# Optimization experiments

Measured on AMD Instinct MI355X. Metric: run time of the kernel, lower is better.

The kernel has to match this reference:

```python
import jax, jax.numpy as jnp
import numpy as np

TOP_K = 8
SCALE = 2.5  # moe_router_scaling_factor
EPS = 1e-20


def setup_inputs() -> dict:
    key = jax.random.key(0)
    k1, k2 = jax.random.split(key)
    B, S, H, E = 4, 4096, 4096, 64
    hidden_states = jax.random.normal(k1, (B, S, H), dtype=jnp.float32)
    gate_weight = jax.random.normal(k2, (E, H), dtype=jnp.float32) * 0.02
    router_bias = jnp.zeros((E,), dtype=jnp.float32)
    return {"hidden_states": hidden_states, "gate_weight": gate_weight, "router_bias": router_bias}


def reference(hidden_states, gate_weight, router_bias):
    B, S, H = hidden_states.shape
    x = hidden_states.reshape(-1, H).astype(jnp.float32)  # [T, H]
    # need_fp32_gate: fp32 matmul against gate weight transpose -> [T, E]
    logits = jnp.einsum('th,eh->te', x, gate_weight.astype(jnp.float32))
    gate_prob = jax.nn.sigmoid(logits)
    biased = gate_prob + router_bias[None, :]
    # topk on bias-shifted probs; weights gathered from UNbiased probs
    _, indices = jax.lax.top_k(biased, TOP_K)                       # [T, K]
    topk_prob = jnp.take_along_axis(gate_prob, indices, axis=1)     # [T, K]
    weights = topk_prob / (jnp.sum(topk_prob, axis=-1, keepdims=True) + EPS)
    weights = weights * SCALE
    return weights, indices
```

## Files before the change

kernel.cpp:

```cpp
#include <hip/hip_runtime.h>
#include <cmath>


typedef float f32x4 __attribute__((ext_vector_type(4)));
typedef short s16x8 __attribute__((ext_vector_type(8)));
typedef unsigned int u32;
typedef u32 u32x4 __attribute__((ext_vector_type(4)));

#define E_DIM 64
#define KC 32
#define CH_BYTES 12288
#define NPART 4
#define HI_OFF (2u << 20)

union V16 { u32x4 u; s16x8 s; };

__device__ __forceinline__ unsigned short f2bf(float f) {
  unsigned u = __float_as_uint(f);
  u += 0x7fffu + ((u >> 16) & 1u);
  return (unsigned short)(u >> 16);
}
__device__ __forceinline__ float bf2f(unsigned short s) {
  return __uint_as_float(((unsigned)s) << 16);
}

__global__ __launch_bounds__(256) void split_w(
    const float* __restrict__ w, unsigned char* __restrict__ w3, int Hdim)
{
  const int kpr = Hdim >> 4;
  const int g = blockIdx.x * 256 + threadIdx.x;
  const int e = g / kpr;
  const int k0 = (g - e * kpr) * 16;
  if (e >= E_DIM) return;

  const float* src = w + (size_t)e * Hdim + k0;
  float f[16];
#pragma unroll
  for (int i = 0; i < 4; ++i) {
    float4 v = *(const float4*)(src + i * 4);
    f[i*4+0] = v.x; f[i*4+1] = v.y; f[i*4+2] = v.z; f[i*4+3] = v.w;
  }
  unsigned short hs[16], ms[16], ls[16];
#pragma unroll
  for (int i = 0; i < 16; ++i) {
    unsigned short h = f2bf(f[i]);
    float r1 = f[i] - bf2f(h);
    unsigned short m = f2bf(r1);
    float r2 = r1 - bf2f(m);
    hs[i] = h; ms[i] = m; ls[i] = f2bf(r2);
  }
  const int c  = k0 >> 5;
  const int n  = e >> 4;
  const int la = (e & 15) + (((k0 & 31) >> 3) << 4);
  unsigned char* base = w3 + (size_t)c * CH_BYTES + n * 1024;

#define STORE_SPLIT(arr, s)                                              \
  do {                                                                   \
    s16x8 pa, pb;                                                        \
    _Pragma("unroll")                                                    \
    for (int j = 0; j < 8; ++j) { pa[j] = (short)arr[j]; pb[j] = (short)arr[8+j]; } \
    *(s16x8*)(base + (s)*4096 + la * 16)        = pa;                    \
    *(s16x8*)(base + (s)*4096 + (la + 16) * 16) = pb;                    \
  } while (0)

  STORE_SPLIT(hs, 0);
  STORE_SPLIT(ms, 1);
  STORE_SPLIT(ls, 2);
#undef STORE_SPLIT
}

__global__ __launch_bounds__(256, 3) void router_mfma(
    const float* __restrict__ x, const unsigned char* __restrict__ w3,
    const float* __restrict__ bias, float* __restrict__ outw,
    float* __restrict__ outi, float* __restrict__ hi_p,
    float* __restrict__ lo_p, int T, int Hdim)
{
  __shared__ __align__(16) unsigned char lds[2][CH_BYTES];

  const int tid  = threadIdx.x;
  const int wid  = tid >> 6;
  const int lane = tid & 63;
  const int lc   = lane & 15;
  const int lq   = lane >> 4;
  const int by   = blockIdx.y;
  const int nch  = Hdim / KC / gridDim.y;
  const int t0   = blockIdx.x * 64;

  const float* xp = x + (size_t)(t0 + wid * 16 + lc) * Hdim
                      + (size_t)by * nch * KC + lq * 8;
  const unsigned char* w3p = w3 + (size_t)by * nch * CH_BYTES;

  f32x4 acc[4], sum_[4], comp[4];
#pragma unroll
  for (int n = 0; n < 4; ++n) {
    acc[n] = (f32x4){0,0,0,0};
    sum_[n] = (f32x4){0,0,0,0};
    comp[n] = (f32x4){0,0,0,0};
  }

#define WAITV2() asm volatile("s_waitcnt vmcnt(2)" ::: "memory")
#define WAITV0() asm volatile("s_waitcnt vmcnt(0)" ::: "memory")
#define BAR()    __builtin_amdgcn_s_barrier()

#define STAGE(c, b)                                                          \
  do {                                                                       \
    const unsigned char* gs = w3p + (size_t)(c) * CH_BYTES + tid * 16;       \
    unsigned char* ld_ = &lds[b][0] + tid * 16;                              \
    _Pragma("unroll")                                                        \
    for (int i = 0; i < 3; ++i)                                              \
      __builtin_amdgcn_global_load_lds(                                      \
          (const __attribute__((address_space(1))) unsigned int*)(gs + i*4096), \
          (__attribute__((address_space(3))) unsigned int*)(ld_ + i*4096),   \
          16, 0, 0);                                                         \
  } while (0)

#define LOADX(c, X)                                                          \
  do {                                                                       \
    X[0] = *(const float4*)(xp + (size_t)(c) * KC);                          \
    X[1] = *(const float4*)(xp + (size_t)(c) * KC + 4);                      \
  } while (0)

#define SPLIT_PAIR(f0, f1, i, AHU, AMU, ALU)                                 \
  do {                                                                       \
    u32 u0_ = __float_as_uint(f0), u1_ = __float_as_uint(f1);                \
    u32 v0_ = u0_ + 0x8000u, v1_ = u1_ + 0x8000u;                            \
    AHU[i] = __builtin_amdgcn_perm(v1_, v0_, 0x07060302u);                   \
    float r0_ = (f0) - __uint_as_float(v0_ & 0xffff0000u);                   \
    float r1_ = (f1) - __uint_as_float(v1_ & 0xffff0000u);                   \
    u32 w0_ = __float_as_uint(r0_) + 0x8000u;                                \
    u32 w1_ = __float_as_uint(r1_) + 0x8000u;                                \
    AMU[i] = __builtin_amdgcn_perm(w1_, w0_, 0x07060302u);                   \
    float s0_ = r0_ - __uint_as_float(w0_ & 0xffff0000u);                    \
    float s1_ = r1_ - __uint_as_float(w1_ & 0xffff0000u);                    \
    u32 y0_ = __float_as_uint(s0_) + 0x8000u;                                \
    u32 y1_ = __float_as_uint(s1_) + 0x8000u;                                \
    ALU[i] = __builtin_amdgcn_perm(y1_, y0_, 0x07060302u);                   \
  } while (0)

#define CONVERT(X)                                                           \
  do {                                                                       \
    V16 ah_, am_, al_;                                                       \
    SPLIT_PAIR(X[0].x, X[0].y, 0, ah_.u, am_.u, al_.u);                      \
    SPLIT_PAIR(X[0].z, X[0].w, 1, ah_.u, am_.u, al_.u);                      \
    SPLIT_PAIR(X[1].x, X[1].y, 2, ah_.u, am_.u, al_.u);                      \
    SPLIT_PAIR(X[1].z, X[1].w, 3, ah_.u, am_.u, al_.u);                      \
    Aah = ah_.s; Aam = am_.s; Aal = al_.s;                                   \
  } while (0)

#define MFMA_ALL(b)                                                          \
  do {                                                                       \
    const unsigned char* B_ = &lds[b][0] + lane * 16;                        \
    __builtin_amdgcn_s_setprio(1);                                           \
    _Pragma("unroll")                                                        \
    for (int g = 0; g < 2; ++g) {                                            \
      s16x8 bh0 = *(const s16x8*)(B_ + 0*4096 + (2*g)*1024);                 \
      s16x8 bh1 = *(const s16x8*)(B_ + 0*4096 + (2*g+1)*1024);               \
      s16x8 bm0 = *(const s16x8*)(B_ + 1*4096 + (2*g)*1024);                 \
      s16x8 bm1 = *(const s16x8*)(B_ + 1*4096 + (2*g+1)*1024);               \
      s16x8 bl0 = *(const s16x8*)(B_ + 2*4096 + (2*g)*1024);                 \
      s16x8 bl1 = *(const s16x8*)(B_ + 2*4096 + (2*g+1)*1024);               \
      acc[2*g]   = __builtin_amdgcn_mfma_f32_16x16x32_bf16(Aah, bh0, acc[2*g],   0,0,0); \
      acc[2*g+1] = __builtin_amdgcn_mfma_f32_16x16x32_bf16(Aah, bh1, acc[2*g+1], 0,0,0); \
      acc[2*g]   = __builtin_amdgcn_mfma_f32_16x16x32_bf16(Aah, bm0, acc[2*g],   0,0,0); \
      acc[2*g+1] = __builtin_amdgcn_mfma_f32_16x16x32_bf16(Aah, bm1, acc[2*g+1], 0,0,0); \
      acc[2*g]   = __builtin_amdgcn_mfma_f32_16x16x32_bf16(Aam, bh0, acc[2*g],   0,0,0); \
      acc[2*g+1] = __builtin_amdgcn_mfma_f32_16x16x32_bf16(Aam, bh1, acc[2*g+1], 0,0,0); \
      acc[2*g]   = __builtin_amdgcn_mfma_f32_16x16x32_bf16(Aah, bl0, acc[2*g],   0,0,0); \
      acc[2*g+1] = __builtin_amdgcn_mfma_f32_16x16x32_bf16(Aah, bl1, acc[2*g+1], 0,0,0); \
      acc[2*g]   = __builtin_amdgcn_mfma_f32_16x16x32_bf16(Aam, bm0, acc[2*g],   0,0,0); \
      acc[2*g+1] = __builtin_amdgcn_mfma_f32_16x16x32_bf16(Aam, bm1, acc[2*g+1], 0,0,0); \
      acc[2*g]   = __builtin_amdgcn_mfma_f32_16x16x32_bf16(Aal, bh0, acc[2*g],   0,0,0); \
      acc[2*g+1] = __builtin_amdgcn_mfma_f32_16x16x32_bf16(Aal, bh1, acc[2*g+1], 0,0,0); \
    }                                                                        \
    __builtin_amdgcn_s_setprio(0);                                           \
  } while (0)

#define FOLD()                                                               \
  do {                                                                       \
    _Pragma("unroll")                                                        \
    for (int n = 0; n < 4; ++n)                                              \
      _Pragma("unroll")                                                      \
      for (int r = 0; r < 4; ++r) {                                          \
        float a_ = acc[n][r];                                                \
        float s_ = sum_[n][r];                                               \
        float t_ = s_ + a_;                                                  \
        float z_ = t_ - s_;                                                  \
        comp[n][r] += (s_ - (t_ - z_)) + (a_ - z_);                          \
        sum_[n][r] = t_;                                                     \
        acc[n][r] = 0.f;                                                     \
      }                                                                      \
  } while (0)

#define ITER_FULL(c, k, XCUR, XN2)                                           \
  do {                                                                       \
    STAGE((c) + 1, ((k) + 1) & 1);                                           \
    LOADX((c) + 2, XN2);                                                     \
    CONVERT(XCUR);                                                           \
    __builtin_amdgcn_sched_barrier(0);                                       \
    MFMA_ALL((k) & 1);                                                       \
    WAITV2();                                                                \
    BAR();                                                                   \
  } while (0)

  float4 X0[2], X1[2], X2[2], X3[2];
  s16x8 Aah, Aam, Aal;

  STAGE(0, 0);
  LOADX(0, X0);
  LOADX(1, X1);
  asm volatile("s_waitcnt vmcnt(4)" ::: "memory");
  BAR();

#pragma unroll 1
  for (int c = 0; c + 4 < nch; c += 4) {
    ITER_FULL(c + 0, 0, X0, X2);
    ITER_FULL(c + 1, 1, X1, X3);
    ITER_FULL(c + 2, 2, X2, X0);
    ITER_FULL(c + 3, 3, X3, X1);
    FOLD();
  }
  {
    const int c = nch - 4;
    ITER_FULL(c + 0, 0, X0, X2);
    ITER_FULL(c + 1, 1, X1, X3);
    STAGE(c + 3, 1);
    CONVERT(X2);
    __builtin_amdgcn_sched_barrier(0);
    MFMA_ALL(0);
    WAITV0();
    BAR();
    CONVERT(X3);
    MFMA_ALL(1);
    FOLD();
  }

  if (gridDim.y != 1) {
#pragma unroll
    for (int n = 0; n < 4; ++n)
#pragma unroll
      for (int r = 0; r < 4; ++r) {
        const int tok = t0 + wid * 16 + lq * 4 + r;
        const size_t o = ((size_t)by * T + tok) * E_DIM + n * 16 + lc;
        hi_p[o] = sum_[n][r];
        lo_p[o] = comp[n][r];
      }
    return;
  }

  float bias_v[4];
#pragma unroll
  for (int n = 0; n < 4; ++n) bias_v[n] = bias[n * 16 + lc];

  float pr[4][4], bi[4][4];
#pragma unroll
  for (int n = 0; n < 4; ++n)
#pragma unroll
    for (int r = 0; r < 4; ++r) {
      float logit = sum_[n][r] + comp[n][r];
      float p = 1.0f / (1.0f + expf(-logit));
      pr[n][r] = p;
      bi[n][r] = p + bias_v[n];
    }
#pragma unroll
  for (int r = 0; r < 4; ++r) {
    float v0 = bi[0][r], v1 = bi[1][r], v2 = bi[2][r], v3 = bi[3][r];
    float p0 = pr[0][r], p1 = pr[1][r], p2 = pr[2][r], p3 = pr[3][r];
    float sum = 0.f, selp = 0.f;
    int seli = 0;
#pragma unroll
    for (int k = 0; k < 8; ++k) {
      float bv = v0; int bn = 0; float bp = p0;
      if (v1 > bv) { bv = v1; bn = 1; bp = p1; }
      if (v2 > bv) { bv = v2; bn = 2; bp = p2; }
      if (v3 > bv) { bv = v3; bn = 3; bp = p3; }
      int be = bn * 16 + lc;
#pragma unroll
      for (int off = 8; off >= 1; off >>= 1) {
        float ov = __shfl_xor(bv, off);
        float op = __shfl_xor(bp, off);
        int   oe = __shfl_xor(be, off);
        if (ov > bv || (ov == bv && oe < be)) { bv = ov; bp = op; be = oe; }
      }
      sum += bp;
      if (lc == k) { selp = bp; seli = be; }
      if (lc == (be & 15)) {
        int gsel = be >> 4;
        if      (gsel == 0) v0 = -1e30f;
        else if (gsel == 1) v1 = -1e30f;
        else if (gsel == 2) v2 = -1e30f;
        else                v3 = -1e30f;
      }
    }
    if (lc < 8) {
      const int tok = t0 + wid * 16 + lq * 4 + r;
      outw[(size_t)tok * 8 + lc] = selp * 2.5f / (sum + 1e-20f);
      outi[(size_t)tok * 8 + lc] = (float)seli;
    }
  }
}

__global__ __launch_bounds__(256) void router_topk(
    const float* __restrict__ hi_p, const float* __restrict__ lo_p,
    const float* __restrict__ bias, float* __restrict__ outw,
    float* __restrict__ outi, int T)
{
  const int lane = threadIdx.x & 63;
  const int t = blockIdx.x * 4 + (threadIdx.x >> 6);
  if (t >= T) return;

  float s = 0.f, c = 0.f, losum = 0.f;
#pragma unroll
  for (int p = 0; p < NPART; ++p) {
    const size_t o = ((size_t)p * T + t) * E_DIM + lane;
    float a = hi_p[o];
    float tt = s + a;
    float z = tt - s;
    c += (s - (tt - z)) + (a - z);
    s = tt;
    losum += lo_p[o];
  }
  const float logit = s + (c + losum);

  const float prob = 1.0f / (1.0f + expf(-logit));
  float v = prob + bias[lane];

  float sum = 0.f, selw = 0.f;
  int seli = 0;
#pragma unroll
  for (int k = 0; k < 8; ++k) {
    float rv = v;
    int   ri = lane;
#pragma unroll
    for (int off = 32; off > 0; off >>= 1) {
      float ov = __shfl_xor(rv, off);
      int   oi = __shfl_xor(ri, off);
      if (ov > rv || (ov == rv && oi < ri)) { rv = ov; ri = oi; }
    }
    float pwin = __shfl(prob, ri);
    sum += pwin;
    if (lane == k)  { selw = pwin; seli = ri; }
    if (lane == ri) v = -INFINITY;
  }

  if (lane < 8) {
    float scale = 2.5f / (sum + 1e-20f);
    outw[(size_t)t * 8 + lane] = selw * scale;
    outi[(size_t)t * 8 + lane] = (float)seli;
  }
}

extern "C" void kernel_launch(void* const* d_in, const int* in_sizes, int n_in,
                              void* d_out, int out_size, void* d_ws, size_t ws_size,
                              hipStream_t stream) {
  const float* x    = (const float*)d_in[0];
  const float* w    = (const float*)d_in[1];
  const float* bias = (const float*)d_in[2];

  const int E    = in_sizes[2];
  const int Hdim = in_sizes[1] / E;
  const int T    = in_sizes[0] / Hdim;

  unsigned char* ws = (unsigned char*)d_ws;
  unsigned char* w3 = ws;
  float* hi_p = (float*)(ws + HI_OFF);
  float* lo_p = hi_p + (size_t)NPART * T * E_DIM;

  const size_t need = (size_t)HI_OFF + (size_t)2 * NPART * T * E_DIM * sizeof(float);
  const int nparts = (ws_size >= need) ? NPART : 1;

  const int nElemGroups = E * Hdim / 16;
  split_w<<<(nElemGroups + 255) / 256, 256, 0, stream>>>(w, w3, Hdim);

  float* outw = (float*)d_out;
  float* outi = outw + (size_t)T * 8;

  dim3 gridG(T / 64, nparts);
  router_mfma<<<gridG, 256, 0, stream>>>(x, w3, bias, outw, outi, hi_p, lo_p, T, Hdim);

  if (nparts != 1) {
    router_topk<<<(T + 3) / 4, 256, 0, stream>>>(hi_p, lo_p, bias, outw, outi, T);
  }
}
```

Baseline: 112.3 us.

## Triple-buffer weight LDS staging, raise occupancy hint, interleave partial sums

The weight-chunk staging goes from two LDS buffers to three, so chunks are prefetched two steps ahead with a looser vmcnt wait. The x register buffers shrink from four to two, and launch bounds now request four blocks per CU instead of three. The hi/lo partial sums are written as float2, interleaved by token and partition, so the top-k kernel reads them contiguously. The 36KB of LDS per block may limit how many blocks actually fit per CU, and tighter register budgets could cause spills.

```diff
diff --git a/kernel.cpp b/kernel.cpp
--- a/kernel.cpp
+++ b/kernel.cpp
@@ -69,13 +69,13 @@
 #undef STORE_SPLIT
 }
 
-__global__ __launch_bounds__(256, 3) void router_mfma(
+__global__ __launch_bounds__(256, 4) void router_mfma(
     const float* __restrict__ x, const unsigned char* __restrict__ w3,
     const float* __restrict__ bias, float* __restrict__ outw,
-    float* __restrict__ outi, float* __restrict__ hi_p,
-    float* __restrict__ lo_p, int T, int Hdim)
+    float* __restrict__ outi, float2* __restrict__ pp,
+    int T, int Hdim)
 {
-  __shared__ __align__(16) unsigned char lds[2][CH_BYTES];
+  __shared__ __align__(16) unsigned char lds[3 * CH_BYTES];
 
   const int tid  = threadIdx.x;
   const int wid  = tid >> 6;
@@ -98,14 +98,15 @@
     comp[n] = (f32x4){0,0,0,0};
   }
 
-#define WAITV2() asm volatile("s_waitcnt vmcnt(2)" ::: "memory")
+#define SB()     __builtin_amdgcn_sched_barrier(0)
+#define WAITV5() asm volatile("s_waitcnt vmcnt(5)" ::: "memory")
 #define WAITV0() asm volatile("s_waitcnt vmcnt(0)" ::: "memory")
 #define BAR()    __builtin_amdgcn_s_barrier()
 
-#define STAGE(c, b)                                                          \
+#define STAGE(c, so)                                                         \
   do {                                                                       \
     const unsigned char* gs = w3p + (size_t)(c) * CH_BYTES + tid * 16;       \
-    unsigned char* ld_ = &lds[b][0] + tid * 16;                              \
+    unsigned char* ld_ = &lds[0] + (so) + tid * 16;                          \
     _Pragma("unroll")                                                        \
     for (int i = 0; i < 3; ++i)                                              \
       __builtin_amdgcn_global_load_lds(                                      \
@@ -147,9 +148,9 @@
     Aah = ah_.s; Aam = am_.s; Aal = al_.s;                                   \
   } while (0)
 
-#define MFMA_ALL(b)                                                          \
-  do {                                                                       \
-    const unsigned char* B_ = &lds[b][0] + lane * 16;                        \
+#define MFMA_ALL(ro)                                                         \
+  do {                                                                       \
+    const unsigned char* B_ = &lds[0] + (ro) + lane * 16;                    \
     __builtin_amdgcn_s_setprio(1);                                           \
     _Pragma("unroll")                                                        \
     for (int g = 0; g < 2; ++g) {                                            \
@@ -191,46 +192,47 @@
       }                                                                      \
   } while (0)
 
-#define ITER_FULL(c, k, XCUR, XN2)                                           \
-  do {                                                                       \
-    STAGE((c) + 1, ((k) + 1) & 1);                                           \
-    LOADX((c) + 2, XN2);                                                     \
-    CONVERT(XCUR);                                                           \
-    __builtin_amdgcn_sched_barrier(0);                                       \
-    MFMA_ALL((k) & 1);                                                       \
-    WAITV2();                                                                \
+#define ITER(c, ro, so, XBUF)                                                \
+  do {                                                                       \
+    STAGE((c) + 2, so);                                                      \
+    CONVERT(XBUF);                                                           \
+    LOADX((c) + 2, XBUF);                                                    \
+    SB();                                                                    \
+    MFMA_ALL(ro);                                                            \
+    WAITV5();                                                                \
     BAR();                                                                   \
   } while (0)
 
-  float4 X0[2], X1[2], X2[2], X3[2];
+  float4 XA[2], XB[2];
   s16x8 Aah, Aam, Aal;
 
-  STAGE(0, 0);
-  LOADX(0, X0);
-  LOADX(1, X1);
-  asm volatile("s_waitcnt vmcnt(4)" ::: "memory");
-  BAR();
+  int ro0 = 0, ro1 = CH_BYTES, ro2 = 2 * CH_BYTES;
+
+  STAGE(0, ro0);
+  STAGE(1, ro1);
+  LOADX(0, XA);
+  LOADX(1, XB);
 
 #pragma unroll 1
-  for (int c = 0; c + 4 < nch; c += 4) {
-    ITER_FULL(c + 0, 0, X0, X2);
-    ITER_FULL(c + 1, 1, X1, X3);
-    ITER_FULL(c + 2, 2, X2, X0);
-    ITER_FULL(c + 3, 3, X3, X1);
+  for (int c = 0; c < nch - 4; c += 4) {
+    ITER(c + 0, ro0, ro2, XA);
+    ITER(c + 1, ro1, ro0, XB);
+    ITER(c + 2, ro2, ro1, XA);
+    ITER(c + 3, ro0, ro2, XB);
     FOLD();
-  }
+    int t_ = ro0; ro0 = ro1; ro1 = ro2; ro2 = t_;
+  }
+  ITER(nch - 4, ro0, ro2, XA);
+  ITER(nch - 3, ro1, ro0, XB);
   {
-    const int c = nch - 4;
-    ITER_FULL(c + 0, 0, X0, X2);
-    ITER_FULL(c + 1, 1, X1, X3);
-    STAGE(c + 3, 1);
-    CONVERT(X2);
-    __builtin_amdgcn_sched_barrier(0);
-    MFMA_ALL(0);
+    CONVERT(XA);
+    SB();
+    MFMA_ALL(ro2);
     WAITV0();
     BAR();
-    CONVERT(X3);
-    MFMA_ALL(1);
+    CONVERT(XB);
+    SB();
+    MFMA_ALL(ro0);
     FOLD();
   }
 
@@ -240,9 +242,8 @@
 #pragma unroll
       for (int r = 0; r < 4; ++r) {
         const int tok = t0 + wid * 16 + lq * 4 + r;
-        const size_t o = ((size_t)by * T + tok) * E_DIM + n * 16 + lc;
-        hi_p[o] = sum_[n][r];
-        lo_p[o] = comp[n][r];
+        const size_t o = ((size_t)tok * NPART + by) * E_DIM + n * 16 + lc;
+        pp[o] = make_float2(sum_[n][r], comp[n][r]);
       }
     return;
   }
@@ -300,9 +301,8 @@
 }
 
 __global__ __launch_bounds__(256) void router_topk(
-    const float* __restrict__ hi_p, const float* __restrict__ lo_p,
-    const float* __restrict__ bias, float* __restrict__ outw,
-    float* __restrict__ outi, int T)
+    const float2* __restrict__ pp, const float* __restrict__ bias,
+    float* __restrict__ outw, float* __restrict__ outi, int T)
 {
   const int lane = threadIdx.x & 63;
   const int t = blockIdx.x * 4 + (threadIdx.x >> 6);
@@ -311,13 +311,13 @@
   float s = 0.f, c = 0.f, losum = 0.f;
 #pragma unroll
   for (int p = 0; p < NPART; ++p) {
-    const size_t o = ((size_t)p * T + t) * E_DIM + lane;
-    float a = hi_p[o];
+    const float2 v = pp[((size_t)t * NPART + p) * E_DIM + lane];
+    float a = v.x;
     float tt = s + a;
     float z = tt - s;
     c += (s - (tt - z)) + (a - z);
     s = tt;
-    losum += lo_p[o];
+    losum += v.y;
   }
   const float logit = s + (c + losum);
 
@@ -362,10 +362,9 @@
 
   unsigned char* ws = (unsigned char*)d_ws;
   unsigned char* w3 = ws;
-  float* hi_p = (float*)(ws + HI_OFF);
-  float* lo_p = hi_p + (size_t)NPART * T * E_DIM;
-
-  const size_t need = (size_t)HI_OFF + (size_t)2 * NPART * T * E_DIM * sizeof(float);
+  float2* pp = (float2*)(ws + HI_OFF);
+
+  const size_t need = (size_t)HI_OFF + (size_t)NPART * T * E_DIM * sizeof(float2);
   const int nparts = (ws_size >= need) ? NPART : 1;
 
   const int nElemGroups = E * Hdim / 16;
@@ -375,9 +374,9 @@
   float* outi = outw + (size_t)T * 8;
 
   dim3 gridG(T / 64, nparts);
-  router_mfma<<<gridG, 256, 0, stream>>>(x, w3, bias, outw, outi, hi_p, lo_p, T, Hdim);
+  router_mfma<<<gridG, 256, 0, stream>>>(x, w3, bias, outw, outi, pp, T, Hdim);
 
   if (nparts != 1) {
-    router_topk<<<(T + 3) / 4, 256, 0, stream>>>(hi_p, lo_p, bias, outw, outi, T);
-  }
-}
+    router_topk<<<(T + 3) / 4, 256, 0, stream>>>(pp, bias, outw, outi, T);
+  }
+}
```

After: 109.9 us. -2.1%, faster.
